# Kernel optimization log

Measured on AMD Instinct MI355X. Metric: run time of the kernel, lower is better.

## Reference

```python
import jax, jax.numpy as jnp
import numpy as np

B, S, D = 32, 256, 768
H = 12
HD = D // H           # 64
MLP = 4 * D           # 3072
EPS = 1e-5


def layernorm(x, g, b):
    mu = jnp.mean(x, axis=-1, keepdims=True)
    var = jnp.mean((x - mu) ** 2, axis=-1, keepdims=True)
    return (x - mu) * jax.lax.rsqrt(var + EPS) * g + b


def setup_inputs() -> dict:
    key = jax.random.key(0)
    ks = jax.random.split(key, 16)
    s_head = 1.0 / np.sqrt(HD)
    s_d = 1.0 / np.sqrt(D)
    s_mlp = 1.0 / np.sqrt(MLP)
    return {
        "x": jax.random.normal(ks[0], (B, S, D), dtype=jnp.float32),
        "g1": jnp.ones((D,), jnp.float32),
        "beta1": jnp.zeros((D,), jnp.float32),
        # per-head linear weights, torch Linear layout [out, in] stacked over heads
        "Wq": jax.random.uniform(ks[1], (H, HD, HD), jnp.float32, -s_head, s_head),
        "bq": jax.random.uniform(ks[2], (H, HD), jnp.float32, -s_head, s_head),
        "Wk": jax.random.uniform(ks[3], (H, HD, HD), jnp.float32, -s_head, s_head),
        "bk": jax.random.uniform(ks[4], (H, HD), jnp.float32, -s_head, s_head),
        "Wv": jax.random.uniform(ks[5], (H, HD, HD), jnp.float32, -s_head, s_head),
        "bv": jax.random.uniform(ks[6], (H, HD), jnp.float32, -s_head, s_head),
        "g2": jnp.ones((D,), jnp.float32),
        "beta2": jnp.zeros((D,), jnp.float32),
        "W1": jax.random.uniform(ks[7], (MLP, D), jnp.float32, -s_d, s_d),
        "bm1": jax.random.uniform(ks[8], (MLP,), jnp.float32, -s_d, s_d),
        "W2": jax.random.uniform(ks[9], (D, MLP), jnp.float32, -s_mlp, s_mlp),
        "bm2": jax.random.uniform(ks[10], (D,), jnp.float32, -s_mlp, s_mlp),
    }


def reference(x, g1, beta1, Wq, bq, Wk, bk, Wv, bv, g2, beta2, W1, bm1, W2, bm2):
    # --- MHA on norm1(x), fused over batch and heads ---
    h = layernorm(x, g1, beta1)                      # [B,S,D]
    hh = h.reshape(B, S, H, HD)                      # head split matches slicing in Mymha
    # q_e = sum_d hh_d * W[e,d]  (torch Linear: y = x @ W.T + b)
    q = jnp.einsum('bshd,hed->bshe', hh, Wq) + bq
    k = jnp.einsum('bshd,hed->bshe', hh, Wk) + bk
    v = jnp.einsum('bshd,hed->bshe', hh, Wv) + bv
    scores = jnp.einsum('bshe,bthe->bhst', q, k) / np.sqrt(HD)
    attn = jax.nn.softmax(scores, axis=-1)           # [B,H,S,S]
    ctx = jnp.einsum('bhst,bthe->bshe', attn, v).reshape(B, S, D)
    out = ctx + x
    # --- MLP on norm2(out) ---
    h2 = layernorm(out, g2, beta2)
    m = jax.nn.gelu(h2 @ W1.T + bm1, approximate=False)  # torch nn.GELU is exact erf
    out = m @ W2.T + bm2 + out
    return out
```

## Files before the change

### kernel.cpp

```cpp
#include <hip/hip_runtime.h>
#include <hip/hip_bf16.h>
#include <math.h>


static constexpr int Bn = 32, Sn = 256, Dn = 768, Hn = 12, HDn = 64, MLPn = 3072;
static constexpr int NT = Bn * Sn;

typedef unsigned short ushort_t;
typedef unsigned int u32;
typedef __attribute__((ext_vector_type(8))) short short8;
typedef __attribute__((ext_vector_type(4))) float f32x4;

__device__ __forceinline__ float bf2f(ushort_t u) { return __uint_as_float(((u32)u) << 16); }
__device__ __forceinline__ ushort_t f2bf(float f) {
  u32 u = __float_as_uint(f);
  u += 0x7fffu + ((u >> 16) & 1u);
  return (ushort_t)(u >> 16);
}

__device__ __forceinline__ void async_cp16(const ushort_t* g, ushort_t* l) {
  __builtin_amdgcn_global_load_lds(
      (const __attribute__((address_space(1))) u32*)g,
      (__attribute__((address_space(3))) u32*)l, 16, 0, 0);
}

__global__ __launch_bounds__(256) void k_prep(
    const float* __restrict__ Wq, const float* __restrict__ Wk,
    const float* __restrict__ Wv, const float* __restrict__ bq,
    const float* __restrict__ bk, const float* __restrict__ bv,
    const float* __restrict__ W1, const float* __restrict__ W2,
    const float* __restrict__ x, const float* __restrict__ g1,
    const float* __restrict__ be1,
    ushort_t* __restrict__ Wc, float* __restrict__ bc,
    ushort_t* __restrict__ W1b, ushort_t* __restrict__ W2b,
    ushort_t* __restrict__ hb)
{
  __shared__ float red[8];
  const int bx = blockIdx.x;
  const int tid = threadIdx.x;
  if (bx < 576) {
    int i = bx * 256 + tid;
    int h = i / 12288, rem = i - h * 12288;
    int mat = rem / 4096, w = rem - mat * 4096;
    const float* src = (mat == 0) ? Wq : ((mat == 1) ? Wk : Wv);
    Wc[i] = f2bf(src[h * 4096 + w]);
    if (i < Hn * 192) {
      int h2 = i / 192, r2 = i - h2 * 192;
      int m2 = r2 / 64, e2 = r2 - m2 * 64;
      const float* bs = (m2 == 0) ? bq : ((m2 == 1) ? bk : bv);
      bc[i] = bs[h2 * 64 + e2];
    }
  } else if (bx < 5184) {
    int j = bx - 576;
    const float* src = (j < 2304) ? W1 : W2;
    ushort_t* dst = (j < 2304) ? W1b : W2b;
    int i = (j % 2304) * 256 + tid;
    float4 v = ((const float4*)src)[i];
    ushort4 o;
    o.x = f2bf(v.x); o.y = f2bf(v.y); o.z = f2bf(v.z); o.w = f2bf(v.w);
    ((ushort4*)dst)[i] = o;
  } else {
    const int t = bx - 5184;
    float xv[3];
#pragma unroll
    for (int i = 0; i < 3; i++) xv[i] = x[(size_t)t * Dn + tid + i * 256];
    float s = xv[0] + xv[1] + xv[2];
#pragma unroll
    for (int off = 32; off > 0; off >>= 1) s += __shfl_down(s, off, 64);
    if ((tid & 63) == 0) red[tid >> 6] = s;
    __syncthreads();
    float mean = (red[0] + red[1] + red[2] + red[3]) * (1.0f / 768.0f);
    float d0 = xv[0] - mean, d1 = xv[1] - mean, d2 = xv[2] - mean;
    float s2 = d0 * d0 + d1 * d1 + d2 * d2;
#pragma unroll
    for (int off = 32; off > 0; off >>= 1) s2 += __shfl_down(s2, off, 64);
    if ((tid & 63) == 0) red[4 + (tid >> 6)] = s2;
    __syncthreads();
    float rstd = rsqrtf((red[4] + red[5] + red[6] + red[7]) * (1.0f / 768.0f) + 1e-5f);
#pragma unroll
    for (int i = 0; i < 3; i++) {
      int d = tid + i * 256;
      hb[(size_t)t * Dn + d] = f2bf((xv[i] - mean) * rstd * g1[d] + be1[d]);
    }
  }
}

__global__ __launch_bounds__(256) void k_qkv(
    const ushort_t* __restrict__ hb,
    const ushort_t* __restrict__ Wc,
    const float* __restrict__ bc,
    ushort_t* __restrict__ qo, ushort_t* __restrict__ ko, ushort_t* __restrict__ vt)
{
  __shared__ __align__(16) ushort_t As[128 * 72];
  __shared__ __align__(16) ushort_t Ws[192 * 72];
  const int blk = blockIdx.x;
  const int half = blk & 1;
  const int bh = blk >> 1;
  const int b_ = bh / Hn, h_ = bh - b_ * Hn;
  const int tid = threadIdx.x;
  const int t0 = b_ * Sn + half * 128;

  {
    int row = tid >> 1, seg = (tid & 1) * 32;
    const uint4* g = (const uint4*)(hb + (size_t)(t0 + row) * Dn + h_ * 64 + seg);
    uint4* s = (uint4*)(As + row * 72 + seg);
    s[0] = g[0]; s[1] = g[1]; s[2] = g[2]; s[3] = g[3];
  }
  {
    int rr = tid >> 2, seg = (tid & 3) * 16;
    const ushort_t* gw = Wc + h_ * 12288;
#pragma unroll
    for (int p = 0; p < 3; p++) {
      int R = p * 64 + rr;
      const uint4* g = (const uint4*)(gw + R * 64 + seg);
      uint4* s = (uint4*)(Ws + R * 72 + seg);
      s[0] = g[0]; s[1] = g[1];
    }
  }
  __syncthreads();

  const int wave = tid >> 6, lane = tid & 63;
  const int wm = (wave >> 1) * 64, wn = (wave & 1) * 96;
  const int lrow = lane & 15, quad = lane >> 4;

  f32x4 acc[4][6];
#pragma unroll
  for (int mi = 0; mi < 4; mi++)
#pragma unroll
    for (int ni = 0; ni < 6; ni++) acc[mi][ni] = (f32x4){0.f, 0.f, 0.f, 0.f};

#pragma unroll
  for (int kk = 0; kk < 2; kk++) {
    short8 af[4], wf[6];
#pragma unroll
    for (int mi = 0; mi < 4; mi++)
      af[mi] = *(const short8*)(As + (wm + mi * 16 + lrow) * 72 + kk * 32 + quad * 8);
#pragma unroll
    for (int ni = 0; ni < 6; ni++)
      wf[ni] = *(const short8*)(Ws + (wn + ni * 16 + lrow) * 72 + kk * 32 + quad * 8);
#pragma unroll
    for (int mi = 0; mi < 4; mi++)
#pragma unroll
      for (int ni = 0; ni < 6; ni++)
        acc[mi][ni] = __builtin_amdgcn_mfma_f32_16x16x32_bf16(af[mi], wf[ni], acc[mi][ni], 0, 0, 0);
  }

#pragma unroll
  for (int ni = 0; ni < 6; ni++) {
    int c = wn + ni * 16 + lrow;
    int mat = c >> 6, e = c & 63;
    float bb = bc[h_ * 192 + c];
    if (mat < 2) {
      ushort_t* dst = (mat == 0) ? qo : ko;
      size_t base = (((size_t)bh) * Sn + half * 128 + wm) * HDn + e;
#pragma unroll
      for (int mi = 0; mi < 4; mi++) {
#pragma unroll
        for (int r = 0; r < 4; r++) {
          int lr = mi * 16 + quad * 4 + r;
          dst[base + (size_t)lr * HDn] = f2bf(acc[mi][ni][r] + bb);
        }
      }
    } else {
      size_t rowb = ((size_t)bh * 64 + e) * Sn + half * 128 + wm + quad * 4;
#pragma unroll
      for (int mi = 0; mi < 4; mi++) {
        ushort4 pk;
        pk.x = f2bf(acc[mi][ni][0] + bb);
        pk.y = f2bf(acc[mi][ni][1] + bb);
        pk.z = f2bf(acc[mi][ni][2] + bb);
        pk.w = f2bf(acc[mi][ni][3] + bb);
        *(ushort4*)(vt + rowb + mi * 16) = pk;
      }
    }
  }
}

__global__ __launch_bounds__(256) void k_attn(
    const ushort_t* __restrict__ q,
    const ushort_t* __restrict__ kg_,
    const ushort_t* __restrict__ vt,
    const float* __restrict__ x,
    float* __restrict__ out1)
{
  __shared__ __align__(16) ushort_t Ks[64 * 72];
  __shared__ __align__(16) ushort_t Vts[64 * 264];
  __shared__ __align__(16) ushort_t Pw[4][16 * 72];
  const int blk = blockIdx.x;
  const int qtr = blk & 3, bh = blk >> 2;
  const int b_ = bh / Hn, h_ = bh - b_ * Hn;
  const int tid = threadIdx.x, wave = tid >> 6, lane = tid & 63;
  const int lr16 = lane & 15, quad = lane >> 4;
  const int s0 = qtr * 64 + wave * 16;

  {
    int r = tid >> 2, cseg = (tid & 3) * 64;
    const uint4* g = (const uint4*)(vt + ((size_t)bh * 64 + r) * Sn + cseg);
    uint4* s = (uint4*)(Vts + r * 264 + cseg);
#pragma unroll
    for (int i = 0; i < 8; i++) s[i] = g[i];
  }

  short8 qf[2];
  {
    const ushort_t* qg = q + ((size_t)bh * Sn + s0 + lr16) * HDn + quad * 8;
    qf[0] = *(const short8*)(qg);
    qf[1] = *(const short8*)(qg + 32);
  }

  f32x4 of[4];
#pragma unroll
  for (int et = 0; et < 4; et++) of[et] = (f32x4){0.f, 0.f, 0.f, 0.f};
  float mrow[4] = {-3.0e38f, -3.0e38f, -3.0e38f, -3.0e38f};
  float lsum[4] = {0.f, 0.f, 0.f, 0.f};

  const ushort_t* kgb = kg_ + (size_t)bh * Sn * HDn;

  for (int c = 0; c < 4; c++) {
    if (c) __syncthreads();
    {
      int row = tid >> 2, seg = (tid & 3) * 16;
      const uint4* g = (const uint4*)(kgb + (size_t)(c * 64 + row) * HDn + seg);
      uint4* s = (uint4*)(Ks + row * 72 + seg);
      s[0] = g[0]; s[1] = g[1];
    }
    __syncthreads();

    f32x4 sc[4];
#pragma unroll
    for (int ni = 0; ni < 4; ni++) sc[ni] = (f32x4){0.f, 0.f, 0.f, 0.f};
#pragma unroll
    for (int kk = 0; kk < 2; kk++) {
#pragma unroll
      for (int ni = 0; ni < 4; ni++) {
        short8 kf = *(const short8*)(Ks + (ni * 16 + lr16) * 72 + kk * 32 + quad * 8);
        sc[ni] = __builtin_amdgcn_mfma_f32_16x16x32_bf16(qf[kk], kf, sc[ni], 0, 0, 0);
      }
    }

    float alpha[4];
#pragma unroll
    for (int r = 0; r < 4; r++) {
      float m_ = fmaxf(fmaxf(sc[0][r], sc[1][r]), fmaxf(sc[2][r], sc[3][r]));
#pragma unroll
      for (int msk = 8; msk >= 1; msk >>= 1) m_ = fmaxf(m_, __shfl_xor(m_, msk, 64));
      float mn = fmaxf(mrow[r], m_);
      alpha[r] = __expf((mrow[r] - mn) * 0.125f);
      mrow[r] = mn;
    }
#pragma unroll
    for (int ni = 0; ni < 4; ni++) {
#pragma unroll
      for (int r = 0; r < 4; r++) {
        float p = __expf((sc[ni][r] - mrow[r]) * 0.125f);
        sc[ni][r] = p;
        Pw[wave][(quad * 4 + r) * 72 + ni * 16 + lr16] = f2bf(p);
      }
    }
#pragma unroll
    for (int r = 0; r < 4; r++) {
      float s_ = (sc[0][r] + sc[1][r]) + (sc[2][r] + sc[3][r]);
#pragma unroll
      for (int msk = 8; msk >= 1; msk >>= 1) s_ += __shfl_xor(s_, msk, 64);
      lsum[r] = lsum[r] * alpha[r] + s_;
    }
#pragma unroll
    for (int et = 0; et < 4; et++)
#pragma unroll
      for (int r = 0; r < 4; r++) of[et][r] *= alpha[r];

    short8 pf0 = *(const short8*)(&Pw[wave][lr16 * 72 + quad * 8]);
    short8 pf1 = *(const short8*)(&Pw[wave][lr16 * 72 + 32 + quad * 8]);
#pragma unroll
    for (int et = 0; et < 4; et++) {
      short8 vf0 = *(const short8*)(Vts + (et * 16 + lr16) * 264 + c * 64 + quad * 8);
      short8 vf1 = *(const short8*)(Vts + (et * 16 + lr16) * 264 + c * 64 + 32 + quad * 8);
      of[et] = __builtin_amdgcn_mfma_f32_16x16x32_bf16(pf0, vf0, of[et], 0, 0, 0);
      of[et] = __builtin_amdgcn_mfma_f32_16x16x32_bf16(pf1, vf1, of[et], 0, 0, 0);
    }
  }

  const size_t obase = ((size_t)b_ * Sn + s0) * Dn + h_ * 64;
#pragma unroll
  for (int r = 0; r < 4; r++) {
    float rl = 1.0f / lsum[r];
    int row = quad * 4 + r;
#pragma unroll
    for (int et = 0; et < 4; et++) {
      size_t idx = obase + (size_t)row * Dn + et * 16 + lr16;
      out1[idx] = of[et][r] * rl + x[idx];
    }
  }
}

__global__ __launch_bounds__(256) void k_ln2(
    const float* __restrict__ in, const float* __restrict__ g2,
    const float* __restrict__ be2, ushort_t* __restrict__ h2)
{
  const int t = blockIdx.x, tid = threadIdx.x;
  __shared__ float red[8];
  float xv[3];
#pragma unroll
  for (int i = 0; i < 3; i++) xv[i] = in[(size_t)t * Dn + tid + i * 256];
  float s = xv[0] + xv[1] + xv[2];
#pragma unroll
  for (int off = 32; off > 0; off >>= 1) s += __shfl_down(s, off, 64);
  if ((tid & 63) == 0) red[tid >> 6] = s;
  __syncthreads();
  float mean = (red[0] + red[1] + red[2] + red[3]) * (1.0f / 768.0f);
  float d0 = xv[0] - mean, d1 = xv[1] - mean, d2 = xv[2] - mean;
  float s2 = d0 * d0 + d1 * d1 + d2 * d2;
#pragma unroll
  for (int off = 32; off > 0; off >>= 1) s2 += __shfl_down(s2, off, 64);
  if ((tid & 63) == 0) red[4 + (tid >> 6)] = s2;
  __syncthreads();
  float rstd = rsqrtf((red[4] + red[5] + red[6] + red[7]) * (1.0f / 768.0f) + 1e-5f);
#pragma unroll
  for (int i = 0; i < 3; i++) {
    int d = tid + i * 256;
    h2[(size_t)t * Dn + d] = f2bf((xv[i] - mean) * rstd * g2[d] + be2[d]);
  }
}

__global__ __launch_bounds__(512, 2) void k_gemm1(
    const ushort_t* __restrict__ A,
    const ushort_t* __restrict__ Bw,
    const float* __restrict__ bias,
    ushort_t* __restrict__ CoutB)
{
  constexpr int KD = Dn;
  constexpr int NTILES = 12;
  __shared__ __align__(16) ushort_t smem[65536];
  const int b = blockIdx.x;
  const int xcd = b & 7, slot = b >> 3;
  const int cc = slot % 12, rloc = slot / 12;
  const int m0 = (xcd * 4 + rloc) * 256, n0 = cc * 256;
  const int tid = threadIdx.x;
  const int wave = tid >> 6, lane = tid & 63;
  const int wm2 = (wave >> 2) * 128, wn2 = (wave & 3) * 64;
  const int lrow = lane & 15, quad = lane >> 4;
  const int key = lrow & 7;

  f32x4 acc[8][4];
#pragma unroll
  for (int mi = 0; mi < 8; mi++)
#pragma unroll
    for (int ni = 0; ni < 4; ni++) acc[mi][ni] = (f32x4){0.f, 0.f, 0.f, 0.f};

  auto stageH = [&](int ht, int part) {
    if (ht >= NTILES) return;
    const int k0 = ht * 64;
    ushort_t* tb = smem + (ht & 1) * 32768 + ((part >= 2) ? 16384 : 0) + (part & 1) * 8192;
    const ushort_t* gs = (part >= 2) ? Bw : A;
    const int gbase = ((part >= 2) ? n0 : m0) + (part & 1) * 128;
#pragma unroll
    for (int j = 0; j < 2; ++j) {
      int q = j * 512 + tid;
      int row = q >> 3;
      int sc = (q & 7) ^ (row & 7);
      async_cp16(gs + (size_t)(gbase + row) * KD + k0 + sc * 8, tb + q * 8);
    }
  };

  stageH(0, 2); stageH(0, 0); stageH(0, 1); stageH(0, 3); stageH(1, 2); stageH(1, 0);
  asm volatile("s_waitcnt vmcnt(4)" ::: "memory");
  __builtin_amdgcn_s_barrier();
  __builtin_amdgcn_sched_barrier(0);

  short8 af[4][2], bl[2][2], bh[2][2];
  for (int t = 0; t < NTILES; ++t) {
    const ushort_t* Ab = smem + (t & 1) * 32768;
    const ushort_t* Bb = Ab + 16384;

#pragma unroll
    for (int mi = 0; mi < 4; ++mi)
#pragma unroll
      for (int kk = 0; kk < 2; ++kk)
        af[mi][kk] = *(const short8*)(Ab + (wm2 + mi * 16 + lrow) * 64 + (((kk << 2) + quad) ^ key) * 8);
#pragma unroll
    for (int ni = 0; ni < 2; ++ni)
#pragma unroll
      for (int kk = 0; kk < 2; ++kk)
        bl[ni][kk] = *(const short8*)(Bb + (wn2 + ni * 16 + lrow) * 64 + (((kk << 2) + quad) ^ key) * 8);
    stageH(t + 1, 1);
    __builtin_amdgcn_s_barrier();
    asm volatile("s_waitcnt lgkmcnt(0)" ::: "memory");
    __builtin_amdgcn_sched_barrier(0);
    __builtin_amdgcn_s_setprio(1);
#pragma unroll
    for (int kk = 0; kk < 2; ++kk)
#pragma unroll
      for (int mi = 0; mi < 4; ++mi)
#pragma unroll
        for (int ni = 0; ni < 2; ++ni)
          acc[mi][ni] = __builtin_amdgcn_mfma_f32_16x16x32_bf16(af[mi][kk], bl[ni][kk], acc[mi][ni], 0, 0, 0);
    __builtin_amdgcn_s_setprio(0);
    __builtin_amdgcn_s_barrier();
    __builtin_amdgcn_sched_barrier(0);

#pragma unroll
    for (int ni = 0; ni < 2; ++ni)
#pragma unroll
      for (int kk = 0; kk < 2; ++kk)
        bh[ni][kk] = *(const short8*)(Bb + (wn2 + 32 + ni * 16 + lrow) * 64 + (((kk << 2) + quad) ^ key) * 8);
    stageH(t + 1, 3);
    __builtin_amdgcn_s_barrier();
    asm volatile("s_waitcnt lgkmcnt(0)" ::: "memory");
    __builtin_amdgcn_sched_barrier(0);
    __builtin_amdgcn_s_setprio(1);
#pragma unroll
    for (int kk = 0; kk < 2; ++kk)
#pragma unroll
      for (int mi = 0; mi < 4; ++mi)
#pragma unroll
        for (int ni = 0; ni < 2; ++ni)
          acc[mi][2 + ni] = __builtin_amdgcn_mfma_f32_16x16x32_bf16(af[mi][kk], bh[ni][kk], acc[mi][2 + ni], 0, 0, 0);
    __builtin_amdgcn_s_setprio(0);
    __builtin_amdgcn_s_barrier();
    __builtin_amdgcn_sched_barrier(0);

#pragma unroll
    for (int mi = 0; mi < 4; ++mi)
#pragma unroll
      for (int kk = 0; kk < 2; ++kk)
        af[mi][kk] = *(const short8*)(Ab + (wm2 + 64 + mi * 16 + lrow) * 64 + (((kk << 2) + quad) ^ key) * 8);
    stageH(t + 2, 2);
    __builtin_amdgcn_s_barrier();
    asm volatile("s_waitcnt lgkmcnt(0)" ::: "memory");
    __builtin_amdgcn_sched_barrier(0);
    __builtin_amdgcn_s_setprio(1);
#pragma unroll
    for (int kk = 0; kk < 2; ++kk)
#pragma unroll
      for (int mi = 0; mi < 4; ++mi)
#pragma unroll
        for (int ni = 0; ni < 2; ++ni)
          acc[4 + mi][2 + ni] = __builtin_amdgcn_mfma_f32_16x16x32_bf16(af[mi][kk], bh[ni][kk], acc[4 + mi][2 + ni], 0, 0, 0);
    __builtin_amdgcn_s_setprio(0);
    __builtin_amdgcn_s_barrier();
    __builtin_amdgcn_sched_barrier(0);

    stageH(t + 2, 0);
    __builtin_amdgcn_s_barrier();
    __builtin_amdgcn_s_setprio(1);
#pragma unroll
    for (int kk = 0; kk < 2; ++kk)
#pragma unroll
      for (int mi = 0; mi < 4; ++mi)
#pragma unroll
        for (int ni = 0; ni < 2; ++ni)
          acc[4 + mi][ni] = __builtin_amdgcn_mfma_f32_16x16x32_bf16(af[mi][kk], bl[ni][kk], acc[4 + mi][ni], 0, 0, 0);
    __builtin_amdgcn_s_setprio(0);
    if (t < NTILES - 2) {
      asm volatile("s_waitcnt vmcnt(4)" ::: "memory");
    } else if (t == NTILES - 2) {
      asm volatile("s_waitcnt vmcnt(0)" ::: "memory");
    }
    __builtin_amdgcn_s_barrier();
    __builtin_amdgcn_sched_barrier(0);
  }

  float bwv[4];
#pragma unroll
  for (int ni = 0; ni < 4; ++ni) bwv[ni] = bias[n0 + wn2 + ni * 16 + lrow];
  __syncthreads();
#pragma unroll
  for (int mi = 0; mi < 8; ++mi) {
#pragma unroll
    for (int ni = 0; ni < 4; ++ni) {
      int col = wn2 + ni * 16 + lrow;
#pragma unroll
      for (int r = 0; r < 4; ++r) {
        int row = wm2 + mi * 16 + quad * 4 + r;
        float vv = acc[mi][ni][r] + bwv[ni];
        float u = vv * (0.7978845608f + 0.0356774081f * vv * vv);
        float o = vv / (1.0f + __expf(-2.0f * u));
        int ck = (col >> 3) ^ ((row >> 2) & 7);
        smem[row * 256 + (ck << 3) + (col & 7)] = f2bf(o);
      }
    }
  }
  __syncthreads();
#pragma unroll
  for (int i = 0; i < 16; ++i) {
    int idx = i * 512 + tid;
    int rr = idx >> 5, ck = idx & 31;
    const uint4 v = *(const uint4*)(smem + rr * 256 + ((ck ^ ((rr >> 2) & 7)) << 3));
    *(uint4*)(CoutB + (size_t)(m0 + rr) * MLPn + n0 + ck * 8) = v;
  }
}

__global__ __launch_bounds__(256) void k_gemm2(
    const ushort_t* __restrict__ A,
    const ushort_t* __restrict__ Bw,
    const float* __restrict__ bias,
    const float* __restrict__ res,
    float* __restrict__ out)
{
  constexpr int KDIM = MLPn, N = Dn;
  __shared__ __align__(16) ushort_t smem[24576];
  ushort_t* As0 = smem;
  ushort_t* Bs0 = smem + 4096;
  ushort_t* As1 = smem + 12288;
  ushort_t* Bs1 = smem + 16384;
  const int b = blockIdx.x;
  const int xcd = b & 7, slot = b >> 3;
  const int cc = slot % 6, rloc = slot / 6;
  const int m0 = (xcd * 16 + rloc) * 64, n0 = cc * 128;
  const int tid = threadIdx.x;
  const int wave = tid >> 6, lane = tid & 63;
  const int wm = (wave >> 1) << 5, wn = (wave & 1) << 6;
  const int lrow = lane & 15, quad = lane >> 4;
  const int r8 = lane >> 3;
  const int c8s = (((lane & 7) ^ ((lane >> 3) & 7))) * 8;
  const int qsw2[2] = { ((0 * 4 + quad) ^ (lrow & 7)) * 8,
                        ((1 * 4 + quad) ^ (lrow & 7)) * 8 };

  f32x4 acc[2][4];
#pragma unroll
  for (int mi = 0; mi < 2; mi++)
#pragma unroll
    for (int ni = 0; ni < 4; ni++) acc[mi][ni] = (f32x4){0.f, 0.f, 0.f, 0.f};

  auto stage = [&](int k0, ushort_t* Ad, ushort_t* Bd) {
    async_cp16(A + (size_t)(m0 + wave * 8 + r8) * KDIM + k0 + c8s,
               Ad + (wave * 8) * 64);
    async_cp16(A + (size_t)(m0 + 32 + wave * 8 + r8) * KDIM + k0 + c8s,
               Ad + (32 + wave * 8) * 64);
#pragma unroll
    for (int g = 0; g < 4; g++)
      async_cp16(Bw + (size_t)(n0 + g * 32 + wave * 8 + r8) * KDIM + k0 + c8s,
                 Bd + (g * 32 + wave * 8) * 64);
  };
  auto compute = [&](const ushort_t* As_, const ushort_t* Bs_) {
#pragma unroll
    for (int kk = 0; kk < 2; kk++) {
      short8 af[2], bfv[4];
#pragma unroll
      for (int mi = 0; mi < 2; mi++)
        af[mi] = *(const short8*)(As_ + (wm + mi * 16 + lrow) * 64 + qsw2[kk]);
#pragma unroll
      for (int ni = 0; ni < 4; ni++)
        bfv[ni] = *(const short8*)(Bs_ + (wn + ni * 16 + lrow) * 64 + qsw2[kk]);
      __builtin_amdgcn_s_setprio(1);
#pragma unroll
      for (int mi = 0; mi < 2; mi++)
#pragma unroll
        for (int ni = 0; ni < 4; ni++)
          acc[mi][ni] = __builtin_amdgcn_mfma_f32_16x16x32_bf16(af[mi], bfv[ni], acc[mi][ni], 0, 0, 0);
      __builtin_amdgcn_s_setprio(0);
    }
  };

  stage(0, As0, Bs0);
  stage(64, As1, Bs1);
  for (int s = 0; s < 46; s += 2) {
    __builtin_amdgcn_sched_barrier(0);
    asm volatile("s_waitcnt vmcnt(6)" ::: "memory");
    __builtin_amdgcn_s_barrier();
    __builtin_amdgcn_sched_barrier(0);
    compute(As0, Bs0);
    __builtin_amdgcn_s_barrier();
    __builtin_amdgcn_sched_barrier(0);
    stage((s + 2) * 64, As0, Bs0);
    __builtin_amdgcn_sched_barrier(0);
    asm volatile("s_waitcnt vmcnt(6)" ::: "memory");
    __builtin_amdgcn_s_barrier();
    __builtin_amdgcn_sched_barrier(0);
    compute(As1, Bs1);
    __builtin_amdgcn_s_barrier();
    __builtin_amdgcn_sched_barrier(0);
    stage((s + 3) * 64, As1, Bs1);
  }
  __builtin_amdgcn_sched_barrier(0);
  asm volatile("s_waitcnt vmcnt(6)" ::: "memory");
  __builtin_amdgcn_s_barrier();
  __builtin_amdgcn_sched_barrier(0);
  compute(As0, Bs0);
  __builtin_amdgcn_sched_barrier(0);
  asm volatile("s_waitcnt vmcnt(0)" ::: "memory");
  __builtin_amdgcn_s_barrier();
  __builtin_amdgcn_sched_barrier(0);
  compute(As1, Bs1);

#pragma unroll
  for (int ni = 0; ni < 4; ni++) {
    int col = n0 + wn + ni * 16 + lrow;
    float bc = bias[col];
#pragma unroll
    for (int mi = 0; mi < 2; mi++) {
#pragma unroll
      for (int r = 0; r < 4; r++) {
        int row = m0 + wm + mi * 16 + quad * 4 + r;
        size_t idx = (size_t)row * N + col;
        out[idx] = acc[mi][ni][r] + bc + res[idx];
      }
    }
  }
}

extern "C" void kernel_launch(void* const* d_in, const int* in_sizes, int n_in,
                              void* d_out, int out_size, void* d_ws, size_t ws_size,
                              hipStream_t stream) {
  (void)in_sizes; (void)n_in; (void)out_size; (void)ws_size;
  const float* x   = (const float*)d_in[0];
  const float* g1  = (const float*)d_in[1];
  const float* be1 = (const float*)d_in[2];
  const float* Wq  = (const float*)d_in[3];
  const float* bq  = (const float*)d_in[4];
  const float* Wk  = (const float*)d_in[5];
  const float* bk  = (const float*)d_in[6];
  const float* Wv  = (const float*)d_in[7];
  const float* bv  = (const float*)d_in[8];
  const float* g2  = (const float*)d_in[9];
  const float* be2 = (const float*)d_in[10];
  const float* W1  = (const float*)d_in[11];
  const float* bm1 = (const float*)d_in[12];
  const float* W2  = (const float*)d_in[13];
  const float* bm2 = (const float*)d_in[14];
  float* outp = (float*)d_out;

  char* ws = (char*)d_ws;
  float*    out1 = (float*)ws;
  ushort_t* hb   = (ushort_t*)ws;
  ushort_t* qb   = (ushort_t*)(ws + 25165824);
  ushort_t* kb   = (ushort_t*)(ws + 37748736);
  ushort_t* vtb  = (ushort_t*)(ws + 50331648);
  ushort_t* h2   = qb;
  ushort_t* mb   = (ushort_t*)(ws + 37748736);
  ushort_t* Wc   = (ushort_t*)(ws + 88080384);
  ushort_t* W1b  = (ushort_t*)(ws + 88375296);
  ushort_t* W2b  = (ushort_t*)(ws + 93093888);
  float*    bcb  = (float*)(ws + 97812480);

  k_prep<<<dim3(5184 + NT), dim3(256), 0, stream>>>(Wq, Wk, Wv, bq, bk, bv, W1, W2,
                                                    x, g1, be1, Wc, bcb, W1b, W2b, hb);
  k_qkv<<<dim3(Bn * Hn * 2), dim3(256), 0, stream>>>(hb, Wc, bcb, qb, kb, vtb);
  k_attn<<<dim3(Bn * Hn * 4), dim3(256), 0, stream>>>(qb, kb, vtb, x, out1);
  k_ln2<<<dim3(NT), dim3(256), 0, stream>>>(out1, g2, be2, h2);
  k_gemm1<<<dim3(384), dim3(512), 0, stream>>>(h2, W1b, bm1, mb);
  k_gemm2<<<dim3(768), dim3(256), 0, stream>>>(mb, W2b, bm2, out1, outp);
}
```

Before: 287.0 us.

## Halve gemm1 K-tile and LDS footprint, restructure pipeline and epilogue in two passes

The MLP up-projection GEMM now uses a 32-wide K tile (24 iterations) instead of 64, cutting the LDS buffer from 128KB to 64KB, and raises the launch-bounds occupancy hint from 2 to 4. The staggered four-phase half-tile staging becomes a simpler two-phase loop that prefetches one full tile ahead and waits on all global loads every iteration. The GELU/bf16 epilogue is split into two passes over 128-row halves so it fits the smaller shared buffer. More occupancy could hide latency, but the shallower prefetch, full vmcnt(0) waits, doubled barrier count and the 128-accumulator register load may limit it.

```diff
diff --git a/kernel.cpp b/kernel.cpp
--- a/kernel.cpp
+++ b/kernel.cpp
@@ -322,15 +322,15 @@
   }
 }
 
-__global__ __launch_bounds__(512, 2) void k_gemm1(
+__global__ __launch_bounds__(512, 4) void k_gemm1(
     const ushort_t* __restrict__ A,
     const ushort_t* __restrict__ Bw,
     const float* __restrict__ bias,
     ushort_t* __restrict__ CoutB)
 {
   constexpr int KD = Dn;
-  constexpr int NTILES = 12;
-  __shared__ __align__(16) ushort_t smem[65536];
+  constexpr int NTILES = 24;
+  __shared__ __align__(16) ushort_t smem[32768];
   const int b = blockIdx.x;
   const int xcd = b & 7, slot = b >> 3;
   const int cc = slot % 12, rloc = slot / 12;
@@ -339,7 +339,7 @@
   const int wave = tid >> 6, lane = tid & 63;
   const int wm2 = (wave >> 2) * 128, wn2 = (wave & 3) * 64;
   const int lrow = lane & 15, quad = lane >> 4;
-  const int key = lrow & 7;
+  const int key = lrow & 3;
 
   f32x4 acc[8][4];
 #pragma unroll
@@ -347,115 +347,65 @@
 #pragma unroll
     for (int ni = 0; ni < 4; ni++) acc[mi][ni] = (f32x4){0.f, 0.f, 0.f, 0.f};
 
-  auto stageH = [&](int ht, int part) {
-    if (ht >= NTILES) return;
-    const int k0 = ht * 64;
-    ushort_t* tb = smem + (ht & 1) * 32768 + ((part >= 2) ? 16384 : 0) + (part & 1) * 8192;
-    const ushort_t* gs = (part >= 2) ? Bw : A;
-    const int gbase = ((part >= 2) ? n0 : m0) + (part & 1) * 128;
+  auto stageT = [&](int t) {
+    if (t >= NTILES) return;
+    const int k0 = t * 32;
+    ushort_t* bufA = smem + (t & 1) * 16384;
+    ushort_t* bufB = bufA + 8192;
 #pragma unroll
     for (int j = 0; j < 2; ++j) {
       int q = j * 512 + tid;
-      int row = q >> 3;
-      int sc = (q & 7) ^ (row & 7);
-      async_cp16(gs + (size_t)(gbase + row) * KD + k0 + sc * 8, tb + q * 8);
+      int row = q >> 2;
+      int sc = (q & 3) ^ (row & 3);
+      async_cp16(A + (size_t)(m0 + row) * KD + k0 + sc * 8, bufA + q * 8);
+      async_cp16(Bw + (size_t)(n0 + row) * KD + k0 + sc * 8, bufB + q * 8);
     }
   };
 
-  stageH(0, 2); stageH(0, 0); stageH(0, 1); stageH(0, 3); stageH(1, 2); stageH(1, 0);
-  asm volatile("s_waitcnt vmcnt(4)" ::: "memory");
+  stageT(0);
+  asm volatile("s_waitcnt vmcnt(0)" ::: "memory");
   __builtin_amdgcn_s_barrier();
   __builtin_amdgcn_sched_barrier(0);
 
-  short8 af[4][2], bl[2][2], bh[2][2];
+  short8 af[4], bf[4];
   for (int t = 0; t < NTILES; ++t) {
-    const ushort_t* Ab = smem + (t & 1) * 32768;
-    const ushort_t* Bb = Ab + 16384;
+    const ushort_t* Ab = smem + (t & 1) * 16384;
+    const ushort_t* Bb = Ab + 8192;
 
 #pragma unroll
     for (int mi = 0; mi < 4; ++mi)
-#pragma unroll
-      for (int kk = 0; kk < 2; ++kk)
-        af[mi][kk] = *(const short8*)(Ab + (wm2 + mi * 16 + lrow) * 64 + (((kk << 2) + quad) ^ key) * 8);
-#pragma unroll
-    for (int ni = 0; ni < 2; ++ni)
-#pragma unroll
-      for (int kk = 0; kk < 2; ++kk)
-        bl[ni][kk] = *(const short8*)(Bb + (wn2 + ni * 16 + lrow) * 64 + (((kk << 2) + quad) ^ key) * 8);
-    stageH(t + 1, 1);
+      af[mi] = *(const short8*)(Ab + (wm2 + mi * 16 + lrow) * 32 + ((quad ^ key) * 8));
+#pragma unroll
+    for (int ni = 0; ni < 4; ++ni)
+      bf[ni] = *(const short8*)(Bb + (wn2 + ni * 16 + lrow) * 32 + ((quad ^ key) * 8));
+    stageT(t + 1);
     __builtin_amdgcn_s_barrier();
     asm volatile("s_waitcnt lgkmcnt(0)" ::: "memory");
     __builtin_amdgcn_sched_barrier(0);
     __builtin_amdgcn_s_setprio(1);
 #pragma unroll
-    for (int kk = 0; kk < 2; ++kk)
-#pragma unroll
-      for (int mi = 0; mi < 4; ++mi)
-#pragma unroll
-        for (int ni = 0; ni < 2; ++ni)
-          acc[mi][ni] = __builtin_amdgcn_mfma_f32_16x16x32_bf16(af[mi][kk], bl[ni][kk], acc[mi][ni], 0, 0, 0);
+    for (int mi = 0; mi < 4; ++mi)
+#pragma unroll
+      for (int ni = 0; ni < 4; ++ni)
+        acc[mi][ni] = __builtin_amdgcn_mfma_f32_16x16x32_bf16(af[mi], bf[ni], acc[mi][ni], 0, 0, 0);
     __builtin_amdgcn_s_setprio(0);
     __builtin_amdgcn_s_barrier();
     __builtin_amdgcn_sched_barrier(0);
 
 #pragma unroll
-    for (int ni = 0; ni < 2; ++ni)
-#pragma unroll
-      for (int kk = 0; kk < 2; ++kk)
-        bh[ni][kk] = *(const short8*)(Bb + (wn2 + 32 + ni * 16 + lrow) * 64 + (((kk << 2) + quad) ^ key) * 8);
-    stageH(t + 1, 3);
+    for (int mi = 0; mi < 4; ++mi)
+      af[mi] = *(const short8*)(Ab + (wm2 + 64 + mi * 16 + lrow) * 32 + ((quad ^ key) * 8));
     __builtin_amdgcn_s_barrier();
     asm volatile("s_waitcnt lgkmcnt(0)" ::: "memory");
     __builtin_amdgcn_sched_barrier(0);
     __builtin_amdgcn_s_setprio(1);
 #pragma unroll
-    for (int kk = 0; kk < 2; ++kk)
-#pragma unroll
-      for (int mi = 0; mi < 4; ++mi)
-#pragma unroll
-        for (int ni = 0; ni < 2; ++ni)
-          acc[mi][2 + ni] = __builtin_amdgcn_mfma_f32_16x16x32_bf16(af[mi][kk], bh[ni][kk], acc[mi][2 + ni], 0, 0, 0);
+    for (int mi = 0; mi < 4; ++mi)
+#pragma unroll
+      for (int ni = 0; ni < 4; ++ni)
+        acc[4 + mi][ni] = __builtin_amdgcn_mfma_f32_16x16x32_bf16(af[mi], bf[ni], acc[4 + mi][ni], 0, 0, 0);
     __builtin_amdgcn_s_setprio(0);
-    __builtin_amdgcn_s_barrier();
-    __builtin_amdgcn_sched_barrier(0);
-
-#pragma unroll
-    for (int mi = 0; mi < 4; ++mi)
-#pragma unroll
-      for (int kk = 0; kk < 2; ++kk)
-        af[mi][kk] = *(const short8*)(Ab + (wm2 + 64 + mi * 16 + lrow) * 64 + (((kk << 2) + quad) ^ key) * 8);
-    stageH(t + 2, 2);
-    __builtin_amdgcn_s_barrier();
-    asm volatile("s_waitcnt lgkmcnt(0)" ::: "memory");
-    __builtin_amdgcn_sched_barrier(0);
-    __builtin_amdgcn_s_setprio(1);
-#pragma unroll
-    for (int kk = 0; kk < 2; ++kk)
-#pragma unroll
-      for (int mi = 0; mi < 4; ++mi)
-#pragma unroll
-        for (int ni = 0; ni < 2; ++ni)
-          acc[4 + mi][2 + ni] = __builtin_amdgcn_mfma_f32_16x16x32_bf16(af[mi][kk], bh[ni][kk], acc[4 + mi][2 + ni], 0, 0, 0);
-    __builtin_amdgcn_s_setprio(0);
-    __builtin_amdgcn_s_barrier();
-    __builtin_amdgcn_sched_barrier(0);
-
-    stageH(t + 2, 0);
-    __builtin_amdgcn_s_barrier();
-    __builtin_amdgcn_s_setprio(1);
-#pragma unroll
-    for (int kk = 0; kk < 2; ++kk)
-#pragma unroll
-      for (int mi = 0; mi < 4; ++mi)
-#pragma unroll
-        for (int ni = 0; ni < 2; ++ni)
-          acc[4 + mi][ni] = __builtin_amdgcn_mfma_f32_16x16x32_bf16(af[mi][kk], bl[ni][kk], acc[4 + mi][ni], 0, 0, 0);
-    __builtin_amdgcn_s_setprio(0);
-    if (t < NTILES - 2) {
-      asm volatile("s_waitcnt vmcnt(4)" ::: "memory");
-    } else if (t == NTILES - 2) {
-      asm volatile("s_waitcnt vmcnt(0)" ::: "memory");
-    }
+    asm volatile("s_waitcnt vmcnt(0)" ::: "memory");
     __builtin_amdgcn_s_barrier();
     __builtin_amdgcn_sched_barrier(0);
   }
@@ -463,30 +413,36 @@
   float bwv[4];
 #pragma unroll
   for (int ni = 0; ni < 4; ++ni) bwv[ni] = bias[n0 + wn2 + ni * 16 + lrow];
-  __syncthreads();
-#pragma unroll
-  for (int mi = 0; mi < 8; ++mi) {
-#pragma unroll
-    for (int ni = 0; ni < 4; ++ni) {
-      int col = wn2 + ni * 16 + lrow;
-#pragma unroll
-      for (int r = 0; r < 4; ++r) {
-        int row = wm2 + mi * 16 + quad * 4 + r;
-        float vv = acc[mi][ni][r] + bwv[ni];
-        float u = vv * (0.7978845608f + 0.0356774081f * vv * vv);
-        float o = vv / (1.0f + __expf(-2.0f * u));
-        int ck = (col >> 3) ^ ((row >> 2) & 7);
-        smem[row * 256 + (ck << 3) + (col & 7)] = f2bf(o);
+  const int wr = wave >> 2;
+#pragma unroll
+  for (int p = 0; p < 2; ++p) {
+    if (wr == p) {
+#pragma unroll
+      for (int mi = 0; mi < 8; ++mi) {
+#pragma unroll
+        for (int ni = 0; ni < 4; ++ni) {
+          int col = wn2 + ni * 16 + lrow;
+#pragma unroll
+          for (int r = 0; r < 4; ++r) {
+            int row = mi * 16 + quad * 4 + r;
+            float vv = acc[mi][ni][r] + bwv[ni];
+            float u = vv * (0.7978845608f + 0.0356774081f * vv * vv);
+            float o = vv / (1.0f + __expf(-2.0f * u));
+            int ck = (col >> 3) ^ ((row >> 2) & 7);
+            smem[row * 256 + (ck << 3) + (col & 7)] = f2bf(o);
+          }
+        }
       }
     }
-  }
-  __syncthreads();
-#pragma unroll
-  for (int i = 0; i < 16; ++i) {
-    int idx = i * 512 + tid;
-    int rr = idx >> 5, ck = idx & 31;
-    const uint4 v = *(const uint4*)(smem + rr * 256 + ((ck ^ ((rr >> 2) & 7)) << 3));
-    *(uint4*)(CoutB + (size_t)(m0 + rr) * MLPn + n0 + ck * 8) = v;
+    __syncthreads();
+#pragma unroll
+    for (int i = 0; i < 8; ++i) {
+      int idx = i * 512 + tid;
+      int rr = idx >> 5, ck = idx & 31;
+      const uint4 v = *(const uint4*)(smem + rr * 256 + ((ck ^ ((rr >> 2) & 7)) << 3));
+      *(uint4*)(CoutB + (size_t)(m0 + p * 128 + rr) * MLPn + n0 + ck * 8) = v;
+    }
+    if (p == 0) __syncthreads();
   }
 }
 
```

Measured after the change: 552.8 us. 92.6% more time.

## Retile MLP up-projection GEMM to 256x192 tiles with 512 blocks

Applied to the files above, without the earlier changes.

Changes the first MLP GEMM from 256x256 output tiles (384 blocks) to 256x192 tiles (512 blocks), so each wave computes 128x48 and the grid fills the 256 CUs in exactly two waves of work. The K-loop pipeline is rebuilt with separate A and B staging, a smaller double buffer, and a full vmcnt(0) wait every iteration instead of the earlier deeper prefetch. The epilogue drops the swizzled LDS layout for a padded stride of 200. The aim is better load balance across CUs, at the cost of more redundant A loads and a shallower, less overlapped pipeline.

```diff
diff --git a/kernel.cpp b/kernel.cpp
--- a/kernel.cpp
+++ b/kernel.cpp
@@ -330,46 +330,57 @@
 {
   constexpr int KD = Dn;
   constexpr int NTILES = 12;
-  __shared__ __align__(16) ushort_t smem[65536];
+  constexpr int BUFU = 28672;
+  __shared__ __align__(16) ushort_t smem[57344];
   const int b = blockIdx.x;
   const int xcd = b & 7, slot = b >> 3;
-  const int cc = slot % 12, rloc = slot / 12;
-  const int m0 = (xcd * 4 + rloc) * 256, n0 = cc * 256;
+  const int cc = slot % 16, rloc = slot / 16;
+  const int m0 = (xcd * 4 + rloc) * 256, n0 = cc * 192;
   const int tid = threadIdx.x;
   const int wave = tid >> 6, lane = tid & 63;
-  const int wm2 = (wave >> 2) * 128, wn2 = (wave & 3) * 64;
+  const int wm2 = (wave >> 2) * 128, wn2 = (wave & 3) * 48;
   const int lrow = lane & 15, quad = lane >> 4;
   const int key = lrow & 7;
 
-  f32x4 acc[8][4];
+  f32x4 acc[8][3];
 #pragma unroll
   for (int mi = 0; mi < 8; mi++)
 #pragma unroll
-    for (int ni = 0; ni < 4; ni++) acc[mi][ni] = (f32x4){0.f, 0.f, 0.f, 0.f};
-
-  auto stageH = [&](int ht, int part) {
-    if (ht >= NTILES) return;
-    const int k0 = ht * 64;
-    ushort_t* tb = smem + (ht & 1) * 32768 + ((part >= 2) ? 16384 : 0) + (part & 1) * 8192;
-    const ushort_t* gs = (part >= 2) ? Bw : A;
-    const int gbase = ((part >= 2) ? n0 : m0) + (part & 1) * 128;
+    for (int ni = 0; ni < 3; ni++) acc[mi][ni] = (f32x4){0.f, 0.f, 0.f, 0.f};
+
+  auto stageA = [&](int t, int half) {
+    if (t >= NTILES) return;
+    const int k0 = t * 64;
+    ushort_t* tb = smem + (t & 1) * BUFU + half * 8192;
 #pragma unroll
     for (int j = 0; j < 2; ++j) {
       int q = j * 512 + tid;
       int row = q >> 3;
       int sc = (q & 7) ^ (row & 7);
-      async_cp16(gs + (size_t)(gbase + row) * KD + k0 + sc * 8, tb + q * 8);
+      async_cp16(A + (size_t)(m0 + half * 128 + row) * KD + k0 + sc * 8, tb + q * 8);
     }
   };
-
-  stageH(0, 2); stageH(0, 0); stageH(0, 1); stageH(0, 3); stageH(1, 2); stageH(1, 0);
-  asm volatile("s_waitcnt vmcnt(4)" ::: "memory");
+  auto stageB = [&](int t) {
+    if (t >= NTILES) return;
+    const int k0 = t * 64;
+    ushort_t* tb = smem + (t & 1) * BUFU + 16384;
+#pragma unroll
+    for (int j = 0; j < 3; ++j) {
+      int q = j * 512 + tid;
+      int row = q >> 3;
+      int sc = (q & 7) ^ (row & 7);
+      async_cp16(Bw + (size_t)(n0 + row) * KD + k0 + sc * 8, tb + q * 8);
+    }
+  };
+
+  stageA(0, 0); stageA(0, 1); stageB(0);
+  asm volatile("s_waitcnt vmcnt(0)" ::: "memory");
   __builtin_amdgcn_s_barrier();
   __builtin_amdgcn_sched_barrier(0);
 
-  short8 af[4][2], bl[2][2], bh[2][2];
+  short8 af[4][2], af2[4][2], bf0[3], bf1[3];
   for (int t = 0; t < NTILES; ++t) {
-    const ushort_t* Ab = smem + (t & 1) * 32768;
+    const ushort_t* Ab = smem + (t & 1) * BUFU;
     const ushort_t* Bb = Ab + 16384;
 
 #pragma unroll
@@ -378,96 +389,77 @@
       for (int kk = 0; kk < 2; ++kk)
         af[mi][kk] = *(const short8*)(Ab + (wm2 + mi * 16 + lrow) * 64 + (((kk << 2) + quad) ^ key) * 8);
 #pragma unroll
-    for (int ni = 0; ni < 2; ++ni)
+    for (int ni = 0; ni < 3; ++ni)
+      bf0[ni] = *(const short8*)(Bb + (wn2 + ni * 16 + lrow) * 64 + ((quad ^ key) * 8));
+    stageA(t + 1, 0);
+    __builtin_amdgcn_s_barrier();
+    asm volatile("s_waitcnt lgkmcnt(0)" ::: "memory");
+    __builtin_amdgcn_sched_barrier(0);
+    __builtin_amdgcn_s_setprio(1);
+#pragma unroll
+    for (int mi = 0; mi < 4; ++mi)
+#pragma unroll
+      for (int ni = 0; ni < 3; ++ni)
+        acc[mi][ni] = __builtin_amdgcn_mfma_f32_16x16x32_bf16(af[mi][0], bf0[ni], acc[mi][ni], 0, 0, 0);
+    __builtin_amdgcn_s_setprio(0);
+    __builtin_amdgcn_s_barrier();
+    __builtin_amdgcn_sched_barrier(0);
+
+#pragma unroll
+    for (int ni = 0; ni < 3; ++ni)
+      bf1[ni] = *(const short8*)(Bb + (wn2 + ni * 16 + lrow) * 64 + (((4 + quad) ^ key) * 8));
+#pragma unroll
+    for (int mi = 0; mi < 4; ++mi)
 #pragma unroll
       for (int kk = 0; kk < 2; ++kk)
-        bl[ni][kk] = *(const short8*)(Bb + (wn2 + ni * 16 + lrow) * 64 + (((kk << 2) + quad) ^ key) * 8);
-    stageH(t + 1, 1);
+        af2[mi][kk] = *(const short8*)(Ab + (wm2 + 64 + mi * 16 + lrow) * 64 + (((kk << 2) + quad) ^ key) * 8);
+    stageA(t + 1, 1);
     __builtin_amdgcn_s_barrier();
     asm volatile("s_waitcnt lgkmcnt(0)" ::: "memory");
     __builtin_amdgcn_sched_barrier(0);
     __builtin_amdgcn_s_setprio(1);
 #pragma unroll
-    for (int kk = 0; kk < 2; ++kk)
-#pragma unroll
-      for (int mi = 0; mi < 4; ++mi)
-#pragma unroll
-        for (int ni = 0; ni < 2; ++ni)
-          acc[mi][ni] = __builtin_amdgcn_mfma_f32_16x16x32_bf16(af[mi][kk], bl[ni][kk], acc[mi][ni], 0, 0, 0);
+    for (int mi = 0; mi < 4; ++mi)
+#pragma unroll
+      for (int ni = 0; ni < 3; ++ni)
+        acc[mi][ni] = __builtin_amdgcn_mfma_f32_16x16x32_bf16(af[mi][1], bf1[ni], acc[mi][ni], 0, 0, 0);
     __builtin_amdgcn_s_setprio(0);
     __builtin_amdgcn_s_barrier();
     __builtin_amdgcn_sched_barrier(0);
 
-#pragma unroll
-    for (int ni = 0; ni < 2; ++ni)
-#pragma unroll
-      for (int kk = 0; kk < 2; ++kk)
-        bh[ni][kk] = *(const short8*)(Bb + (wn2 + 32 + ni * 16 + lrow) * 64 + (((kk << 2) + quad) ^ key) * 8);
-    stageH(t + 1, 3);
-    __builtin_amdgcn_s_barrier();
-    asm volatile("s_waitcnt lgkmcnt(0)" ::: "memory");
+    stageB(t + 1);
+    __builtin_amdgcn_s_barrier();
     __builtin_amdgcn_sched_barrier(0);
     __builtin_amdgcn_s_setprio(1);
 #pragma unroll
-    for (int kk = 0; kk < 2; ++kk)
-#pragma unroll
-      for (int mi = 0; mi < 4; ++mi)
-#pragma unroll
-        for (int ni = 0; ni < 2; ++ni)
-          acc[mi][2 + ni] = __builtin_amdgcn_mfma_f32_16x16x32_bf16(af[mi][kk], bh[ni][kk], acc[mi][2 + ni], 0, 0, 0);
+    for (int mi = 0; mi < 4; ++mi)
+#pragma unroll
+      for (int ni = 0; ni < 3; ++ni)
+        acc[4 + mi][ni] = __builtin_amdgcn_mfma_f32_16x16x32_bf16(af2[mi][0], bf0[ni], acc[4 + mi][ni], 0, 0, 0);
     __builtin_amdgcn_s_setprio(0);
     __builtin_amdgcn_s_barrier();
     __builtin_amdgcn_sched_barrier(0);
 
+    __builtin_amdgcn_s_setprio(1);
 #pragma unroll
     for (int mi = 0; mi < 4; ++mi)
 #pragma unroll
-      for (int kk = 0; kk < 2; ++kk)
-        af[mi][kk] = *(const short8*)(Ab + (wm2 + 64 + mi * 16 + lrow) * 64 + (((kk << 2) + quad) ^ key) * 8);
-    stageH(t + 2, 2);
-    __builtin_amdgcn_s_barrier();
-    asm volatile("s_waitcnt lgkmcnt(0)" ::: "memory");
-    __builtin_amdgcn_sched_barrier(0);
-    __builtin_amdgcn_s_setprio(1);
-#pragma unroll
-    for (int kk = 0; kk < 2; ++kk)
-#pragma unroll
-      for (int mi = 0; mi < 4; ++mi)
-#pragma unroll
-        for (int ni = 0; ni < 2; ++ni)
-          acc[4 + mi][2 + ni] = __builtin_amdgcn_mfma_f32_16x16x32_bf16(af[mi][kk], bh[ni][kk], acc[4 + mi][2 + ni], 0, 0, 0);
+      for (int ni = 0; ni < 3; ++ni)
+        acc[4 + mi][ni] = __builtin_amdgcn_mfma_f32_16x16x32_bf16(af2[mi][1], bf1[ni], acc[4 + mi][ni], 0, 0, 0);
     __builtin_amdgcn_s_setprio(0);
-    __builtin_amdgcn_s_barrier();
-    __builtin_amdgcn_sched_barrier(0);
-
-    stageH(t + 2, 0);
-    __builtin_amdgcn_s_barrier();
-    __builtin_amdgcn_s_setprio(1);
-#pragma unroll
-    for (int kk = 0; kk < 2; ++kk)
-#pragma unroll
-      for (int mi = 0; mi < 4; ++mi)
-#pragma unroll
-        for (int ni = 0; ni < 2; ++ni)
-          acc[4 + mi][ni] = __builtin_amdgcn_mfma_f32_16x16x32_bf16(af[mi][kk], bl[ni][kk], acc[4 + mi][ni], 0, 0, 0);
-    __builtin_amdgcn_s_setprio(0);
-    if (t < NTILES - 2) {
-      asm volatile("s_waitcnt vmcnt(4)" ::: "memory");
-    } else if (t == NTILES - 2) {
-      asm volatile("s_waitcnt vmcnt(0)" ::: "memory");
-    }
-    __builtin_amdgcn_s_barrier();
-    __builtin_amdgcn_sched_barrier(0);
-  }
-
-  float bwv[4];
-#pragma unroll
-  for (int ni = 0; ni < 4; ++ni) bwv[ni] = bias[n0 + wn2 + ni * 16 + lrow];
+    asm volatile("s_waitcnt vmcnt(0)" ::: "memory");
+    __builtin_amdgcn_s_barrier();
+    __builtin_amdgcn_sched_barrier(0);
+  }
+
+  float bwv[3];
+#pragma unroll
+  for (int ni = 0; ni < 3; ++ni) bwv[ni] = bias[n0 + wn2 + ni * 16 + lrow];
   __syncthreads();
 #pragma unroll
   for (int mi = 0; mi < 8; ++mi) {
 #pragma unroll
-    for (int ni = 0; ni < 4; ++ni) {
+    for (int ni = 0; ni < 3; ++ni) {
       int col = wn2 + ni * 16 + lrow;
 #pragma unroll
       for (int r = 0; r < 4; ++r) {
@@ -475,17 +467,16 @@
         float vv = acc[mi][ni][r] + bwv[ni];
         float u = vv * (0.7978845608f + 0.0356774081f * vv * vv);
         float o = vv / (1.0f + __expf(-2.0f * u));
-        int ck = (col >> 3) ^ ((row >> 2) & 7);
-        smem[row * 256 + (ck << 3) + (col & 7)] = f2bf(o);
+        smem[row * 200 + col] = f2bf(o);
       }
     }
   }
   __syncthreads();
 #pragma unroll
-  for (int i = 0; i < 16; ++i) {
+  for (int i = 0; i < 12; ++i) {
     int idx = i * 512 + tid;
-    int rr = idx >> 5, ck = idx & 31;
-    const uint4 v = *(const uint4*)(smem + rr * 256 + ((ck ^ ((rr >> 2) & 7)) << 3));
+    int rr = idx / 24, ck = idx - rr * 24;
+    const uint4 v = *(const uint4*)(smem + rr * 200 + ck * 8);
     *(uint4*)(CoutB + (size_t)(m0 + rr) * MLPn + n0 + ck * 8) = v;
   }
 }
@@ -638,6 +629,6 @@
   k_qkv<<<dim3(Bn * Hn * 2), dim3(256), 0, stream>>>(hb, Wc, bcb, qb, kb, vtb);
   k_attn<<<dim3(Bn * Hn * 4), dim3(256), 0, stream>>>(qb, kb, vtb, x, out1);
   k_ln2<<<dim3(NT), dim3(256), 0, stream>>>(out1, g2, be2, h2);
-  k_gemm1<<<dim3(384), dim3(512), 0, stream>>>(h2, W1b, bm1, mb);
+  k_gemm1<<<dim3(512), dim3(512), 0, stream>>>(h2, W1b, bm1, mb);
   k_gemm2<<<dim3(768), dim3(256), 0, stream>>>(mb, W2b, bm2, out1, outp);
 }
```

Result: faster. 277.9 us (-3.2%).
